# Kernel tuning notes

Hardware: AMD Instinct MI355X
Metric: run time of the kernel (lower is better)

## Reference

```python
import jax, jax.numpy as jnp
import numpy as np

HEADS = 8
C = 256            # in_channels == out_channels
NUM_STAR = 4
G = 32             # num graphs
N = 100000         # num nodes
LN_EPS = 1e-5


def setup_inputs() -> dict:
    key = jax.random.key(0)
    ks = jax.random.split(key, 9)
    stars = jax.random.normal(ks[0], (G, NUM_STAR, C), jnp.float32)
    nodes = jax.random.normal(ks[1], (N, C), jnp.float32)
    batch = jnp.sort(jax.random.randint(ks[2], (N,), 0, G))
    s = 1.0 / np.sqrt(C).astype(np.float32)
    Wq_w = jax.random.normal(ks[3], (C, C), jnp.float32) * s
    Wk_w = jax.random.normal(ks[4], (C, C), jnp.float32) * s
    Wv_w = jax.random.normal(ks[5], (C, C), jnp.float32) * s
    Wq_b = jnp.zeros((C,), jnp.float32)
    Wk_b = jnp.zeros((C,), jnp.float32)
    Wv_b = jnp.zeros((C,), jnp.float32)
    ln_gamma = jnp.ones((C,), jnp.float32)
    ln_beta = jnp.zeros((C,), jnp.float32)
    return dict(stars=stars, nodes=nodes, batch=batch,
                Wq_w=Wq_w, Wq_b=Wq_b, Wk_w=Wk_w, Wk_b=Wk_b,
                Wv_w=Wv_w, Wv_b=Wv_b, ln_gamma=ln_gamma, ln_beta=ln_beta)


def reference(stars, nodes, batch, Wq_w, Wq_b, Wk_w, Wk_b, Wv_w, Wv_b, ln_gamma, ln_beta):
    g, num_star, c = stars.shape
    n = nodes.shape[0]
    h = HEADS
    dh = c // h
    s_total = g * num_star                       # number of star nodes
    num_seg = n + s_total

    # x = [nodes; flattened stars]  (star index of (graph gidx, star i) = n + num_star*gidx + i)
    x = jnp.concatenate([nodes, stars.reshape(-1, c)], axis=0)     # [n+S, c]
    q = (x @ Wq_w.T + Wq_b).reshape(-1, h, dh)
    k = (x @ Wk_w.T + Wk_b).reshape(-1, h, dh)
    v = (x @ Wv_w.T + Wv_b).reshape(-1, h, dh)

    # edges: every node -> each of its graph's stars, plus star self-loops (use_star=True)
    rows = (n + num_star * batch[None, :] + jnp.arange(num_star)[:, None]).reshape(-1)  # [num_star*n]
    cols = jnp.broadcast_to(jnp.arange(n), (num_star, n)).reshape(-1)
    star_idx = jnp.arange(n, n + s_total)
    ei = jnp.concatenate([rows, star_idx])       # targets (query side)
    ej = jnp.concatenate([cols, star_idx])       # sources (key/value side)

    qe = q[ei]                                   # [E, h, dh]
    ke = k[ej]
    ve = v[ej]

    score = jnp.einsum('ehd,ehd->eh', qe, ke) / np.sqrt(dh).astype(np.float32)

    # segment softmax over target index (PyG-style, +1e-16 in denominator)
    m = jax.ops.segment_max(score, ei, num_segments=num_seg)
    m = jnp.where(jnp.isfinite(m), m, 0.0)       # empty segments -> 0
    ex = jnp.exp(score - m[ei])
    denom = jax.ops.segment_sum(ex, ei, num_segments=num_seg)
    coef = ex / (denom[ei] + 1e-16)              # [E, h]

    # dropout is identity in eval mode
    out = jax.ops.segment_sum(ve * coef[:, :, None], ei, num_segments=num_seg)  # [n+S, h, dh]
    new_stars = out[n:].reshape(g, num_star, c)

    new_stars = jax.nn.elu(new_stars)            # activation
    new_stars = new_stars + stars                # residual

    mu = jnp.mean(new_stars, axis=-1, keepdims=True)
    var = jnp.mean(jnp.square(new_stars - mu), axis=-1, keepdims=True)
    new_stars = (new_stars - mu) / jnp.sqrt(var + LN_EPS) * ln_gamma + ln_beta
    return new_stars
```

## Files before the change

### kernel.cpp

```cpp
#include <hip/hip_runtime.h>
#include <math.h>

#define HEADS 8
#define C 256
#define NUM_STAR 4
#define SLOTS 32
#define RSQRT_DH 0.17677669529663688f
#define LN_EPS 1e-5f
#define PF 24
#define NT 16
#define FS 260
#define ES 24

typedef __attribute__((ext_vector_type(8))) short short8;
typedef __attribute__((ext_vector_type(4))) float floatx4;

typedef const unsigned int __attribute__((address_space(1)))* gp1_t;
typedef unsigned int __attribute__((address_space(3)))* lp3_t;

__device__ __forceinline__ unsigned int f2b(float f) {
    unsigned int u = __float_as_uint(f);
    return (u + 0x7fffu + ((u >> 16) & 1u)) >> 16;
}
__device__ __forceinline__ unsigned int pk_bf16(float lo, float hi) {
    unsigned int r;
    asm("v_cvt_pk_bf16_f32 %0, %1, %2" : "=v"(r) : "v"(lo), "v"(hi));
    return r;
}
__device__ __forceinline__ void gld_lds16(const float* g, float* l) {
    __builtin_amdgcn_global_load_lds((gp1_t)(const void*)g, (lp3_t)(void*)l, 16, 0, 0);
}
__device__ __forceinline__ void block_sync_lds() {
    asm volatile("s_waitcnt lgkmcnt(0)" ::: "memory");
    __builtin_amdgcn_sched_barrier(0);
    __builtin_amdgcn_s_barrier();
    __builtin_amdgcn_sched_barrier(0);
}

__global__ void k_star_prep(const float* __restrict__ stars,
                            const float* __restrict__ Wq_w, const float* __restrict__ Wq_b,
                            const float* __restrict__ Wk_w, const float* __restrict__ Wk_b,
                            unsigned short* __restrict__ U16, float* __restrict__ eself,
                            float* __restrict__ denom,
                            const int* __restrict__ batch, int N, int G,
                            int* __restrict__ gstart) {
    if (blockIdx.x == gridDim.x - 1) {
        int g = threadIdx.x;
        if (g > G) return;
        if (g == 0) { gstart[0] = 0; return; }
        if (g == G) { gstart[G] = N; return; }
        int lo = 0, hi = N;
        while (lo < hi) {
            int mid = (lo + hi) >> 1;
            if (batch[mid] < g) lo = mid + 1; else hi = mid;
        }
        gstart[g] = lo;
        return;
    }

    __shared__ float xs[C];
    __shared__ float qv[C];
    __shared__ float kv[C];
    const int gs = blockIdx.x;
    const int g = gs >> 2, s = gs & 3;
    const int t = threadIdx.x;

    xs[t] = stars[gs * C + t];
    __syncthreads();

    float aq = Wq_b[t], ak = Wk_b[t];
    const float* wq = Wq_w + (size_t)t * C;
    const float* wk = Wk_w + (size_t)t * C;
    #pragma unroll 4
    for (int j = 0; j < C; j += 4) {
        float4 x4 = *(const float4*)(xs + j);
        float4 a4 = *(const float4*)(wq + j);
        aq += a4.x * x4.x + a4.y * x4.y + a4.z * x4.z + a4.w * x4.w;
        float4 b4 = *(const float4*)(wk + j);
        ak += b4.x * x4.x + b4.y * x4.y + b4.z * x4.z + b4.w * x4.w;
    }
    qv[t] = aq; kv[t] = ak;
    __syncthreads();

    {
        float p = qv[t] * kv[t];
        #pragma unroll
        for (int off = 16; off; off >>= 1) p += __shfl_down(p, off, 32);
        if ((t & 31) == 0) {
            int h = t >> 5;
            float e = __expf(p * RSQRT_DH);
            eself[g * SLOTS + s * HEADS + h] = e;
            denom[g * SLOTS + s * HEADS + h] = e;
        }
    }

    {
        const int c = t;
        #pragma unroll
        for (int h = 0; h < HEADS; ++h) {
            float u = 0.f;
            #pragma unroll
            for (int d = 0; d < 32; ++d)
                u += Wk_w[(size_t)(h * 32 + d) * C + c] * qv[h * 32 + d];
            U16[((size_t)g * SLOTS + s * HEADS + h) * C + c] =
                (unsigned short)f2b(u * RSQRT_DH);
        }
    }
}

__global__ __launch_bounds__(256, 3)
void k_fused(const float* __restrict__ nodes, const unsigned short* __restrict__ U16,
             const int* __restrict__ gstart, float* __restrict__ denom,
             float* __restrict__ Ypart) {
    __shared__ float          fbuf[3 * NT * FS];
    __shared__ unsigned short e_lds[SLOTS * ES];

    const int g = blockIdx.x / PF, pb = blockIdx.x % PF;
    const int t = threadIdx.x;
    const int wv = t >> 6;
    const int l  = t & 63;
    const int lr = l & 15;
    const int q  = l >> 4;

    const int glo = gstart[g], ghi = gstart[g + 1];
    const int len = ghi - glo;
    const int L = (len + PF - 1) / PF;
    const int lo = glo + pb * L;
    const int hi = min(lo + L, ghi);
    const int nr = (hi > lo) ? (hi - lo + NT - 1) / NT : 0;

    const floatx4 z4 = {0.f, 0.f, 0.f, 0.f};
    floatx4 yacc[2][4];
    #pragma unroll
    for (int a = 0; a < 2; ++a)
        #pragma unroll
        for (int b = 0; b < 4; ++b) yacc[a][b] = z4;

    if (nr > 0) {
        short8 ureg[8];
        if (wv < 2) {
            const unsigned short* ug = U16 + (size_t)g * SLOTS * C;
            #pragma unroll
            for (int kt = 0; kt < 8; ++kt)
                ureg[kt] = *(const short8*)&ug[(wv * 16 + lr) * C + q * 8 + kt * 32];
        }
        asm volatile("s_waitcnt vmcnt(0)" ::: "memory");

        float dsum[4];
        #pragma unroll
        for (int i = 0; i < 4; ++i) dsum[i] = 0.f;

        auto issue = [&](int r) {
            const int slot = r % 3;
            #pragma unroll
            for (int i = 0; i < 4; ++i) {
                int node = wv * 4 + i;
                int gn = lo + r * NT + node;
                if (gn >= hi) gn = lo;
                gld_lds16(nodes + (size_t)gn * C + l * 4,
                          &fbuf[(slot * NT + node) * FS]);
            }
        };

        issue(0);
        issue(1);

        for (int rd = 0; rd < nr; ++rd) {
            block_sync_lds();
            issue(rd + 2);
            asm volatile("s_waitcnt vmcnt(8)" ::: "memory");
            __builtin_amdgcn_sched_barrier(0);
            __builtin_amdgcn_s_barrier();

            const float* fb = &fbuf[(rd % 3) * NT * FS];

            if (wv < 2) {
                floatx4 sacc = z4;
                const float* xr = fb + lr * FS + q * 8;
                #pragma unroll
                for (int kt = 0; kt < 8; ++kt) {
                    float4 a4 = *(const float4*)(xr + kt * 32);
                    float4 b4 = *(const float4*)(xr + kt * 32 + 4);
                    short8 bx;
                    ((unsigned int*)&bx)[0] = pk_bf16(a4.x, a4.y);
                    ((unsigned int*)&bx)[1] = pk_bf16(a4.z, a4.w);
                    ((unsigned int*)&bx)[2] = pk_bf16(b4.x, b4.y);
                    ((unsigned int*)&bx)[3] = pk_bf16(b4.z, b4.w);
                    sacc = __builtin_amdgcn_mfma_f32_16x16x32_bf16(ureg[kt], bx, sacc, 0, 0, 0);
                }
                const bool valid = (lo + rd * NT + lr) < hi;
                #pragma unroll
                for (int r = 0; r < 4; ++r) {
                    float ev = valid ? __expf(sacc[r]) : 0.f;
                    dsum[r] += ev;
                    e_lds[(wv * 16 + q * 4 + r) * ES + lr] = (unsigned short)f2b(ev);
                }
            }
            block_sync_lds();

            short8 pa0, pa1;
            if (l < 32) {
                pa0 = *(const short8*)&e_lds[lr * ES + q * 8];
                pa1 = *(const short8*)&e_lds[(16 + lr) * ES + q * 8];
            } else {
                #pragma unroll
                for (int j = 0; j < 8; ++j) { pa0[j] = 0; pa1[j] = 0; }
            }
            #pragma unroll
            for (int ct = 0; ct < 4; ++ct) {
                short8 bx;
                if (l < 32) {
                    const float* col = fb + q * 8 * FS + wv * 64 + ct * 16 + lr;
                    ((unsigned int*)&bx)[0] = pk_bf16(col[0 * FS], col[1 * FS]);
                    ((unsigned int*)&bx)[1] = pk_bf16(col[2 * FS], col[3 * FS]);
                    ((unsigned int*)&bx)[2] = pk_bf16(col[4 * FS], col[5 * FS]);
                    ((unsigned int*)&bx)[3] = pk_bf16(col[6 * FS], col[7 * FS]);
                } else {
                    #pragma unroll
                    for (int j = 0; j < 8; ++j) bx[j] = 0;
                }
                yacc[0][ct] = __builtin_amdgcn_mfma_f32_16x16x32_bf16(pa0, bx, yacc[0][ct], 0, 0, 0);
                yacc[1][ct] = __builtin_amdgcn_mfma_f32_16x16x32_bf16(pa1, bx, yacc[1][ct], 0, 0, 0);
            }
        }

        if (wv < 2) {
            #pragma unroll
            for (int i = 0; i < 4; ++i) {
                float v = dsum[i];
                v += __shfl_xor(v, 1);
                v += __shfl_xor(v, 2);
                v += __shfl_xor(v, 4);
                v += __shfl_xor(v, 8);
                dsum[i] = v;
            }
            if (lr == 0) {
                #pragma unroll
                for (int r = 0; r < 4; ++r)
                    atomicAdd(&denom[g * SLOTS + wv * 16 + q * 4 + r], dsum[r]);
            }
        }
    }

    {
        float* yg = &Ypart[(((size_t)g * PF + pb) * SLOTS) * C];
        #pragma unroll
        for (int st = 0; st < 2; ++st)
            #pragma unroll
            for (int ct = 0; ct < 4; ++ct)
                #pragma unroll
                for (int r = 0; r < 4; ++r)
                    yg[(st * 16 + q * 4 + r) * C + wv * 64 + ct * 16 + lr] = yacc[st][ct][r];
    }
}

__global__ void k_epilogue(const float* __restrict__ stars,
                           const float* __restrict__ Wv_w, const float* __restrict__ Wv_b,
                           const float* __restrict__ gamma, const float* __restrict__ beta,
                           const float* __restrict__ Ypart, const float* __restrict__ eself,
                           const float* __restrict__ denom, float* __restrict__ out) {
    __shared__ float xs[C];
    __shared__ float yl[HEADS * C];
    __shared__ float cs[HEADS], ivd[HEADS], scl[HEADS];
    __shared__ float rb[8];

    const int gs = blockIdx.x;
    const int g = gs >> 2, s = gs & 3;
    const int t = threadIdx.x;

    xs[t] = stars[gs * C + t];
    if (t < HEADS) {
        float dn = denom[g * SLOTS + s * HEADS + t];
        float iv = 1.f / (dn + 1e-16f);
        ivd[t] = iv;
        cs[t] = eself[g * SLOTS + s * HEADS + t] * iv;
        scl[t] = dn * iv;
    }
    __syncthreads();

    for (int i = t; i < HEADS * C; i += 256) {
        int h = i >> 8, j = i & 255;
        float sum = 0.f;
        #pragma unroll
        for (int pbi = 0; pbi < PF; ++pbi)
            sum += Ypart[(((size_t)g * PF + pbi) * SLOTS + s * HEADS + h) * C + j];
        yl[i] = sum * ivd[h] + cs[h] * xs[j];
    }
    __syncthreads();

    const int c = t, h = c >> 5;
    float a = 0.f;
    const float* wv = Wv_w + (size_t)c * C;
    const float* yh = &yl[h * C];
    #pragma unroll 4
    for (int j = 0; j < C; j += 4) {
        float4 w4 = *(const float4*)(wv + j);
        float4 y4 = *(const float4*)(yh + j);
        a += w4.x * y4.x + w4.y * y4.y + w4.z * y4.z + w4.w * y4.w;
    }
    a += Wv_b[c] * scl[h];

    float v = a > 0.f ? a : (__expf(a) - 1.f);
    float r = v + xs[c];

    float ssum = r;
    #pragma unroll
    for (int off = 32; off; off >>= 1) ssum += __shfl_down(ssum, off, 64);
    const int wid = t >> 6, lane = t & 63;
    if (lane == 0) rb[wid] = ssum;
    __syncthreads();
    const float mu = (rb[0] + rb[1] + rb[2] + rb[3]) * (1.f / 256.f);
    const float d = r - mu;
    float vsum = d * d;
    #pragma unroll
    for (int off = 32; off; off >>= 1) vsum += __shfl_down(vsum, off, 64);
    if (lane == 0) rb[4 + wid] = vsum;
    __syncthreads();
    const float var = (rb[4] + rb[5] + rb[6] + rb[7]) * (1.f / 256.f);
    out[gs * C + c] = d * rsqrtf(var + LN_EPS) * gamma[c] + beta[c];
}

extern "C" void kernel_launch(void* const* d_in, const int* in_sizes, int n_in,
                              void* d_out, int out_size, void* d_ws, size_t ws_size,
                              hipStream_t stream) {
    const float* stars = (const float*)d_in[0];
    const float* nodes = (const float*)d_in[1];
    const int*   batch = (const int*)d_in[2];
    const float* Wq_w  = (const float*)d_in[3];
    const float* Wq_b  = (const float*)d_in[4];
    const float* Wk_w  = (const float*)d_in[5];
    const float* Wk_b  = (const float*)d_in[6];
    const float* Wv_w  = (const float*)d_in[7];
    const float* Wv_b  = (const float*)d_in[8];
    const float* gamma = (const float*)d_in[9];
    const float* beta  = (const float*)d_in[10];

    const int N = in_sizes[1] / C;
    const int G = in_sizes[0] / (NUM_STAR * C);

    unsigned short* U16 = (unsigned short*)d_ws;
    float* eself = (float*)((char*)d_ws + (size_t)G * SLOTS * C * 2);
    float* denom = eself + (size_t)G * SLOTS;
    float* Ypart = denom + (size_t)G * SLOTS;
    int*   gstart = (int*)(Ypart + (size_t)G * PF * SLOTS * C);

    float* out = (float*)d_out;

    k_star_prep<<<G * NUM_STAR + 1, 256, 0, stream>>>(stars, Wq_w, Wq_b, Wk_w, Wk_b,
                                                      U16, eself, denom,
                                                      batch, N, G, gstart);
    k_fused<<<G * PF, 256, 0, stream>>>(nodes, U16, gstart, denom, Ypart);
    k_epilogue<<<G * NUM_STAR, 256, 0, stream>>>(stars, Wv_w, Wv_b, gamma, beta,
                                                 Ypart, eself, denom, out);
}
```

Measured before the change: 71.35 us.

## Double node tile to 32 rows so all four waves share score MFMAs

Raises the per-round node tile from 16 to 32 rows so all four waves compute scores (two slot halves × two node groups) instead of only two waves. The full 32-wide K dimension of the aggregation MFMA is now used, where before half the lanes fed zeros. It also moves from triple to double buffering with the next load issued at the end of each round, cuts blocks per graph from 24 to 16, and lowers launch occupancy to 2 blocks per CU. The aims are less idle MFMA work and fewer barriers per node. In exchange there is less prefetch depth and fewer resident blocks to hide memory latency.

```diff
diff --git a/kernel.cpp b/kernel.cpp
--- a/kernel.cpp
+++ b/kernel.cpp
@@ -7,10 +7,10 @@
 #define SLOTS 32
 #define RSQRT_DH 0.17677669529663688f
 #define LN_EPS 1e-5f
-#define PF 24
-#define NT 16
+#define PF 16
+#define NT 32
 #define FS 260
-#define ES 24
+#define EP2 40
 
 typedef __attribute__((ext_vector_type(8))) short short8;
 typedef __attribute__((ext_vector_type(4))) float floatx4;
@@ -108,12 +108,12 @@
     }
 }
 
-__global__ __launch_bounds__(256, 3)
+__global__ __launch_bounds__(256, 2)
 void k_fused(const float* __restrict__ nodes, const unsigned short* __restrict__ U16,
              const int* __restrict__ gstart, float* __restrict__ denom,
              float* __restrict__ Ypart) {
-    __shared__ float          fbuf[3 * NT * FS];
-    __shared__ unsigned short e_lds[SLOTS * ES];
+    __shared__ float          fbuf[2][NT][FS];
+    __shared__ unsigned short el[SLOTS * EP2];
 
     const int g = blockIdx.x / PF, pb = blockIdx.x % PF;
     const int t = threadIdx.x;
@@ -121,13 +121,15 @@
     const int l  = t & 63;
     const int lr = l & 15;
     const int q  = l >> 4;
+    const int st = wv & 1;
+    const int ng = wv >> 1;
 
     const int glo = gstart[g], ghi = gstart[g + 1];
     const int len = ghi - glo;
-    const int L = (len + PF - 1) / PF;
-    const int lo = glo + pb * L;
-    const int hi = min(lo + L, ghi);
-    const int nr = (hi > lo) ? (hi - lo + NT - 1) / NT : 0;
+    const int Lb = (len + PF - 1) / PF;
+    const int blo = glo + pb * Lb;
+    const int bhi = min(blo + Lb, ghi);
+    const int nrw = (bhi > blo) ? (bhi - blo + NT - 1) / NT : 0;
 
     const floatx4 z4 = {0.f, 0.f, 0.f, 0.f};
     floatx4 yacc[2][4];
@@ -135,48 +137,44 @@
     for (int a = 0; a < 2; ++a)
         #pragma unroll
         for (int b = 0; b < 4; ++b) yacc[a][b] = z4;
-
-    if (nr > 0) {
+    float dsum[4];
+    #pragma unroll
+    for (int i = 0; i < 4; ++i) dsum[i] = 0.f;
+
+    if (nrw > 0) {
         short8 ureg[8];
-        if (wv < 2) {
+        {
             const unsigned short* ug = U16 + (size_t)g * SLOTS * C;
             #pragma unroll
             for (int kt = 0; kt < 8; ++kt)
-                ureg[kt] = *(const short8*)&ug[(wv * 16 + lr) * C + q * 8 + kt * 32];
+                ureg[kt] = *(const short8*)&ug[(st * 16 + lr) * C + q * 8 + kt * 32];
         }
         asm volatile("s_waitcnt vmcnt(0)" ::: "memory");
 
-        float dsum[4];
-        #pragma unroll
-        for (int i = 0; i < 4; ++i) dsum[i] = 0.f;
-
         auto issue = [&](int r) {
-            const int slot = r % 3;
-            #pragma unroll
-            for (int i = 0; i < 4; ++i) {
-                int node = wv * 4 + i;
-                int gn = lo + r * NT + node;
-                if (gn >= hi) gn = lo;
-                gld_lds16(nodes + (size_t)gn * C + l * 4,
-                          &fbuf[(slot * NT + node) * FS]);
+            const int buf = r & 1;
+            #pragma unroll
+            for (int i = 0; i < 8; ++i) {
+                int row = wv * 8 + i;
+                int gn = blo + r * NT + row;
+                if (gn >= bhi) gn = blo;
+                gld_lds16(nodes + (size_t)gn * C + l * 4, &fbuf[buf][row][0]);
             }
         };
 
         issue(0);
         issue(1);
 
-        for (int rd = 0; rd < nr; ++rd) {
-            block_sync_lds();
-            issue(rd + 2);
+        for (int rd = 0; rd < nrw; ++rd) {
+            const int cur = rd & 1;
             asm volatile("s_waitcnt vmcnt(8)" ::: "memory");
             __builtin_amdgcn_sched_barrier(0);
             __builtin_amdgcn_s_barrier();
-
-            const float* fb = &fbuf[(rd % 3) * NT * FS];
-
-            if (wv < 2) {
-                floatx4 sacc = z4;
-                const float* xr = fb + lr * FS + q * 8;
+            __builtin_amdgcn_sched_barrier(0);
+
+            floatx4 sacc = z4;
+            {
+                const float* xr = &fbuf[cur][ng * 16 + lr][q * 8];
                 #pragma unroll
                 for (int kt = 0; kt < 8; ++kt) {
                     float4 a4 = *(const float4*)(xr + kt * 32);
@@ -188,69 +186,65 @@
                     ((unsigned int*)&bx)[3] = pk_bf16(b4.z, b4.w);
                     sacc = __builtin_amdgcn_mfma_f32_16x16x32_bf16(ureg[kt], bx, sacc, 0, 0, 0);
                 }
-                const bool valid = (lo + rd * NT + lr) < hi;
+            }
+            {
+                const bool valid = (blo + rd * NT + ng * 16 + lr) < bhi;
                 #pragma unroll
                 for (int r = 0; r < 4; ++r) {
                     float ev = valid ? __expf(sacc[r]) : 0.f;
                     dsum[r] += ev;
-                    e_lds[(wv * 16 + q * 4 + r) * ES + lr] = (unsigned short)f2b(ev);
+                    el[(st * 16 + q * 4 + r) * EP2 + ng * 16 + lr] = (unsigned short)f2b(ev);
                 }
             }
             block_sync_lds();
 
-            short8 pa0, pa1;
-            if (l < 32) {
-                pa0 = *(const short8*)&e_lds[lr * ES + q * 8];
-                pa1 = *(const short8*)&e_lds[(16 + lr) * ES + q * 8];
-            } else {
+            {
+                short8 pa0 = *(const short8*)&el[lr * EP2 + q * 8];
+                short8 pa1 = *(const short8*)&el[(16 + lr) * EP2 + q * 8];
                 #pragma unroll
-                for (int j = 0; j < 8; ++j) { pa0[j] = 0; pa1[j] = 0; }
-            }
-            #pragma unroll
-            for (int ct = 0; ct < 4; ++ct) {
-                short8 bx;
-                if (l < 32) {
-                    const float* col = fb + q * 8 * FS + wv * 64 + ct * 16 + lr;
+                for (int ct = 0; ct < 4; ++ct) {
+                    const int c = wv * 64 + ct * 16 + lr;
+                    short8 bx;
+                    const float* col = &fbuf[cur][q * 8][c];
                     ((unsigned int*)&bx)[0] = pk_bf16(col[0 * FS], col[1 * FS]);
                     ((unsigned int*)&bx)[1] = pk_bf16(col[2 * FS], col[3 * FS]);
                     ((unsigned int*)&bx)[2] = pk_bf16(col[4 * FS], col[5 * FS]);
                     ((unsigned int*)&bx)[3] = pk_bf16(col[6 * FS], col[7 * FS]);
-                } else {
-                    #pragma unroll
-                    for (int j = 0; j < 8; ++j) bx[j] = 0;
+                    yacc[0][ct] = __builtin_amdgcn_mfma_f32_16x16x32_bf16(pa0, bx, yacc[0][ct], 0, 0, 0);
+                    yacc[1][ct] = __builtin_amdgcn_mfma_f32_16x16x32_bf16(pa1, bx, yacc[1][ct], 0, 0, 0);
                 }
-                yacc[0][ct] = __builtin_amdgcn_mfma_f32_16x16x32_bf16(pa0, bx, yacc[0][ct], 0, 0, 0);
-                yacc[1][ct] = __builtin_amdgcn_mfma_f32_16x16x32_bf16(pa1, bx, yacc[1][ct], 0, 0, 0);
             }
-        }
-
-        if (wv < 2) {
-            #pragma unroll
-            for (int i = 0; i < 4; ++i) {
-                float v = dsum[i];
-                v += __shfl_xor(v, 1);
-                v += __shfl_xor(v, 2);
-                v += __shfl_xor(v, 4);
-                v += __shfl_xor(v, 8);
-                dsum[i] = v;
-            }
-            if (lr == 0) {
-                #pragma unroll
-                for (int r = 0; r < 4; ++r)
-                    atomicAdd(&denom[g * SLOTS + wv * 16 + q * 4 + r], dsum[r]);
-            }
+            block_sync_lds();
+            issue(rd + 2);
+        }
+
+        asm volatile("s_waitcnt vmcnt(0)" ::: "memory");
+
+        #pragma unroll
+        for (int i = 0; i < 4; ++i) {
+            float v = dsum[i];
+            v += __shfl_xor(v, 1);
+            v += __shfl_xor(v, 2);
+            v += __shfl_xor(v, 4);
+            v += __shfl_xor(v, 8);
+            dsum[i] = v;
+        }
+        if (lr == 0) {
+            #pragma unroll
+            for (int r = 0; r < 4; ++r)
+                atomicAdd(&denom[g * SLOTS + st * 16 + q * 4 + r], dsum[r]);
         }
     }
 
     {
         float* yg = &Ypart[(((size_t)g * PF + pb) * SLOTS) * C];
         #pragma unroll
-        for (int st = 0; st < 2; ++st)
+        for (int st2 = 0; st2 < 2; ++st2)
             #pragma unroll
             for (int ct = 0; ct < 4; ++ct)
                 #pragma unroll
                 for (int r = 0; r < 4; ++r)
-                    yg[(st * 16 + q * 4 + r) * C + wv * 64 + ct * 16 + lr] = yacc[st][ct][r];
+                    yg[(st2 * 16 + q * 4 + r) * C + wv * 64 + ct * 16 + lr] = yacc[st2][ct][r];
     }
 }
 
```

Measured after the change: 68.36 us. 1.04x faster.
